# Optimization experiments

Measured on AMD Instinct MI355X. Metric: run time of the kernel, lower is better.

## Reference

```python
import jax, jax.numpy as jnp
import numpy as np

# Workspace layout (static slice bounds, per init_kwargs)
SS, SE = 0, 512        # spoke
HPS, HPE = 512, 768    # hub private
HSS, HSE = 768, 1024   # hub shared
TS, TE = 1024, 1088    # tag
HS, HE = 512, 1024     # full hub (priv + shared) for the read path

B, T, D_STATE, D_MODEL, D_LATENT = 8, 4096, 1088, 1024, 128


def setup_inputs() -> dict:
    key = jax.random.key(0)
    ks = jax.random.split(key, 10)
    scale = 0.02  # typical init scale for learned projections
    return {
        "S": jax.random.normal(ks[0], (B, T, D_STATE), jnp.float32),
        "w_spoke": jax.random.normal(ks[1], (B, T, SE - SS), jnp.float32),
        "w_hub_priv": jax.random.normal(ks[2], (B, T, HPE - HPS), jnp.float32),
        "w_hub_shared": jax.random.normal(ks[3], (B, T, HSE - HSS), jnp.float32),
        "tag": jax.random.normal(ks[4], (B, T, TE - TS), jnp.float32),
        "W_read": jax.random.normal(ks[5], (D_MODEL, D_STATE), jnp.float32) * scale,
        "cache": jnp.zeros((B, T, D_LATENT), jnp.float32),
        "latent": jax.random.normal(ks[6], (B, T, D_LATENT), jnp.float32),
        "Wk": jax.random.normal(ks[7], (D_MODEL, D_LATENT), jnp.float32) * scale,
        "Wv": jax.random.normal(ks[8], (D_MODEL, D_LATENT), jnp.float32) * scale,
    }


def reference(S, w_spoke, w_hub_priv, w_hub_shared, tag, W_read, cache, latent, Wk, Wv):
    # --- fused_workspace_write: four independent slice-adds into S ---
    S = S.at[:, :, SS:SE].add(w_spoke)
    S = S.at[:, :, HPS:HPE].add(w_hub_priv)
    S = S.at[:, :, HSS:HSE].add(w_hub_shared)
    S = S.at[:, :, TS:TE].add(tag)

    # --- fused_workspace_read: concat(spoke, hub, tag) then F.linear(., W_read) ---
    readable = jnp.concatenate(
        [S[:, :, SS:SE], S[:, :, HS:HE], S[:, :, TS:TE]], axis=-1
    )  # (B, T, D_STATE)
    out = jnp.einsum("btr,dr->btd", readable, W_read)  # (B, T, D_MODEL)

    # --- CWTLatentCache.update: overwrite latents at start_position=0 ---
    cache = jax.lax.dynamic_update_slice(cache, latent, (0, 0, 0))

    # --- K/V reconstruction from compressed latents via up-projections ---
    k = jnp.einsum("btl,dl->btd", cache, Wk)  # (B, T, D_MODEL)
    v = jnp.einsum("btl,dl->btd", cache, Wv)  # (B, T, D_MODEL)
    return (out, k, v)
```

## Files before the change

kernel.cpp:

```cpp
#include <hip/hip_runtime.h>

typedef __attribute__((ext_vector_type(8))) _Float16 half8;
typedef __attribute__((ext_vector_type(2))) __fp16 half2r;
typedef __attribute__((ext_vector_type(4))) float f32x4;

#define AS1 __attribute__((address_space(1)))
#define AS3 __attribute__((address_space(3)))

union H2U { half2r h; unsigned int u; };
union Frag { half8 v; unsigned long long d[2]; };

__device__ __forceinline__ unsigned int pk(float a, float b) {
    H2U x; x.h = __builtin_amdgcn_cvt_pkrtz(a, b); return x.u;
}

__device__ __forceinline__ void gload_lds16(const void* g, void* l) {
    __builtin_amdgcn_global_load_lds((const AS1 unsigned int*)g,
                                     (AS3 unsigned int*)l, 16, 0, 0);
}

#define WS2_OFF 2228224
#define WS2_SZ  524288
#define W2_ROWB 256
#define A16_SZ  71303168ull

__device__ __forceinline__ void pick_w(int ks, const float* wsp, const float* whp,
                                       const float* whs, const float* wtg,
                                       const float*& wbase, int& wstr, int& wko) {
    if (ks < 8)       { wbase = wsp; wstr = 512; wko = ks * 64; }
    else if (ks < 12) { wbase = whp; wstr = 256; wko = ks * 64 - 512; }
    else if (ks < 16) { wbase = whs; wstr = 256; wko = ks * 64 - 768; }
    else              { wbase = wtg; wstr = 64;  wko = 0; }
}

__device__ __forceinline__ size_t pf_addr(int r, int kt) {
    int kh = kt >> 5, k32 = kt & 31;
    int u = (k32 & 15) >> 2, pos8 = (k32 >> 4) << 3;
    return ((size_t)r << 7) + ((size_t)((((kh << 2) | u) ^ (r & 7)) << 4)) + pos8;
}

__global__ __launch_bounds__(256) void prep_w(const float* __restrict__ Wk,
                                              const float* __restrict__ Wv,
                                              char* __restrict__ ws) {
    int j = blockIdx.x * 256 + threadIdx.x;
    int r = j >> 5;
    int k = (j & 31) << 2;
    const float* src = (r < 1024) ? (Wk + (size_t)r * 128 + k)
                                  : (Wv + (size_t)(r - 1024) * 128 + k);
    f32x4 w = *(const f32x4*)src;
    uint2 q; q.x = pk(w.x, w.y); q.y = pk(w.z, w.w);
    size_t off = WS2_OFF + (size_t)r * W2_ROWB + ((k >> 6) << 7)
               + (((k & 63) << 1) ^ ((r & 7) << 4));
    *(uint2*)(ws + off) = q;
}

__device__ __forceinline__
void fuse_body(int u, const float* __restrict__ S, const float* __restrict__ wsp,
               const float* __restrict__ whp, const float* __restrict__ whs,
               const float* __restrict__ wtg, char* __restrict__ a16) {
    int row = u / 272;
    int rem = u % 272;
    int ks = rem >> 4;
    int k4 = (rem & 15) << 2;

    const float* wbase; int wstr, wko;
    pick_w(ks, wsp, whp, whs, wtg, wbase, wstr, wko);

    f32x4 s4 = *(const f32x4*)(S + (size_t)row * 1088 + ks * 64 + k4);
    f32x4 w4 = *(const f32x4*)(wbase + (size_t)row * wstr + wko + k4);
    uint2 q; q.x = pk(s4.x + w4.x, s4.y + w4.y);
             q.y = pk(s4.z + w4.z, s4.w + w4.w);
    size_t off = ((size_t)((row >> 7) * 17 + ks) << 14) + pf_addr(row & 127, k4);
    *(uint2*)(a16 + off) = q;
}

__device__ __forceinline__
void kv_body(int mblk, int nb, const float* __restrict__ lat,
             const char* __restrict__ ws2, float* __restrict__ outk,
             float* __restrict__ outv, char* lds) {
    char* Al = lds;
    char* Bl = lds + 16384;

    int m0 = mblk << 7;
    int nrow0 = nb << 7;
    float* out = (nb < 8) ? outk : outv;
    int n0 = (nb & 7) << 7;

    int tid = threadIdx.x;
    int lane = tid & 63, wid = tid >> 6;
    int wm = (wid >> 1) << 6, wn = (wid & 1) << 6;
    int lp = lane & 15, lg = lane >> 4;

    f32x4 acc[4][4] = {};

    for (int ks = 0; ks < 2; ++ks) {
        __syncthreads();
        {
            const char* wrow = ws2 + (size_t)nrow0 * W2_ROWB + ks * 128;
            #pragma unroll
            for (int c = 0; c < 4; ++c) {
                int s = c * 4096 + wid * 1024 + lane * 16;
                int n = s >> 7, cb = s & 127;
                gload_lds16(wrow + (size_t)n * W2_ROWB + cb,
                            Bl + c * 4096 + wid * 1024);
            }
        }
        #pragma unroll
        for (int i = 0; i < 8; ++i) {
            int u = i * 256 + tid;
            int row = u >> 4;
            int k4 = (u & 15) << 2;
            f32x4 s4 = *(const f32x4*)(lat + (size_t)(m0 + row) * 128 + ks * 64 + k4);
            uint2 q; q.x = pk(s4.x, s4.y); q.y = pk(s4.z, s4.w);
            *(uint2*)(Al + (row << 7) + ((k4 << 1) ^ ((row & 7) << 4))) = q;
        }
        __syncthreads();

        #pragma unroll
        for (int b = 0; b < 2; ++b) {
            Frag af[4], bf[4];
            #pragma unroll
            for (int f = 0; f < 4; ++f) {
                int ra = wm + f * 16 + lp;  int xa = (ra & 7) << 4;
                af[f].d[0] = *(const unsigned long long*)(Al + (ra << 7) + ((b * 64 + lg * 8) ^ xa));
                af[f].d[1] = *(const unsigned long long*)(Al + (ra << 7) + ((b * 64 + 32 + lg * 8) ^ xa));
                int rb = wn + f * 16 + lp;  int xb = (rb & 7) << 4;
                bf[f].d[0] = *(const unsigned long long*)(Bl + (rb << 7) + ((b * 64 + lg * 8) ^ xb));
                bf[f].d[1] = *(const unsigned long long*)(Bl + (rb << 7) + ((b * 64 + 32 + lg * 8) ^ xb));
            }
            #pragma unroll
            for (int i = 0; i < 4; ++i)
                #pragma unroll
                for (int j = 0; j < 4; ++j)
                    acc[i][j] = __builtin_amdgcn_mfma_f32_16x16x32_f16(af[i].v, bf[j].v, acc[i][j], 0, 0, 0);
        }
    }

    #pragma unroll
    for (int i = 0; i < 4; ++i)
        #pragma unroll
        for (int j = 0; j < 4; ++j) {
            int row = m0 + wm + i * 16 + (lg << 2);
            int col = n0 + wn + j * 16 + lp;
            float* p = out + (size_t)row * 1024 + col;
            #pragma unroll
            for (int r = 0; r < 4; ++r) p[(size_t)r * 1024] = acc[i][j][r];
        }
}

__global__ __launch_bounds__(256, 3)
void fuse_kv(const float* __restrict__ S, const float* __restrict__ wsp,
             const float* __restrict__ whp, const float* __restrict__ whs,
             const float* __restrict__ wtg, char* __restrict__ a16,
             const float* __restrict__ lat, const char* __restrict__ ws2,
             float* __restrict__ outk, float* __restrict__ outv,
             const float* __restrict__ Wr, char* __restrict__ ws,
             int kvpg, int gsz, int nmain) {
    __shared__ char lds[32768];
    int bid = blockIdx.x;
    if (bid >= nmain) {
        int id = (bid - nmain) * 256 + threadIdx.x;
        int n = id / 272;
        int k = (id % 272) * 4;
        f32x4 w = *(const f32x4*)(Wr + (size_t)n * 1088 + k);
        uint2 q; q.x = pk(w.x, w.y); q.y = pk(w.z, w.w);
        int t = k >> 6;
        size_t off = ((size_t)((n >> 7) * 17 + t) << 14) + pf_addr(n & 127, k & 63);
        *(uint2*)(ws + off) = q;
        return;
    }
    int g = bid / gsz, slot = bid - g * gsz;
    if (slot < 17) {
        fuse_body((g * 17 + slot) * 256 + threadIdx.x, S, wsp, whp, whs, wtg, a16);
    } else {
        int idx = g * kvpg + (slot - 17);
        int mblk, nb;
        if (kvpg == 2) { int wg = (idx & 7) * 512 + (idx >> 3); mblk = wg >> 4; nb = wg & 15; }
        else           { int wg = (idx & 7) * 256 + (idx >> 3); mblk = wg >> 3; nb = wg & 7; }
        kv_body(mblk, nb, lat, ws2, outk, outv, lds);
    }
}

__global__ __launch_bounds__(256, 3)
void gemm_v(const float* __restrict__ lat, const char* __restrict__ ws2,
            float* __restrict__ outk, float* __restrict__ outv) {
    __shared__ char lds[32768];
    int idx = blockIdx.x;
    int wg = (idx & 7) * 256 + (idx >> 3);
    kv_body(wg >> 3, 8 + (wg & 7), lat, ws2, outk, outv, lds);
}

__global__ __launch_bounds__(512, 2)
void gemm_read(const char* __restrict__ a16, const char* __restrict__ wws,
               float* __restrict__ out) {
    extern __shared__ char lds[];

    int bid = blockIdx.x;
    int wg   = (bid & 7) * 64 + (bid >> 3);
    int mblk = wg >> 2, nblk = wg & 3;
    int m0 = mblk << 8, n0 = nblk << 8;

    int tid = threadIdx.x;
    int lane = tid & 63, wid = tid >> 6;
    int wm = (wid >> 2) << 7, wn = (wid & 3) << 6;
    int lp = lane & 15, lg = lane >> 4;

    int aoff = (wid >> 2) * 16384;
    int boff = 32768 + (wn >> 7) * 16384;
    int cb64 = wn & 64;

    const char* srcH[4];
    srcH[0] = a16 + ((size_t)((m0 >> 7) * 17) << 14);
    srcH[1] = srcH[0] + (17 << 14);
    srcH[2] = wws + ((size_t)((n0 >> 7) * 17) << 14);
    srcH[3] = srcH[2] + (17 << 14);

    f32x4 acc[8][4] = {};
    Frag af[4], bf[4];

#define STAGE(T, H, DB) do {                                               \
        const char* s_ = srcH[H] + ((size_t)(T) << 14);                    \
        char* d_ = lds + (DB) + (H) * 16384;                               \
        gload_lds16(s_ + tid * 16, d_ + tid * 16);                         \
        gload_lds16(s_ + 8192 + tid * 16, d_ + 8192 + tid * 16);           \
    } while (0)

#define LOADA(MH, KH, BB) do {                                             \
        _Pragma("unroll")                                                  \
        for (int f = 0; f < 4; ++f) {                                      \
            int r_ = (MH) * 64 + f * 16 + lp;                              \
            af[f] = *(const Frag*)(lds + (BB) + aoff + (r_ << 7)           \
                     + ((((((KH) << 2) | lg) ^ (r_ & 7))) << 4));          \
        }                                                                  \
    } while (0)

#define LOADB(KH, BB) do {                                                 \
        _Pragma("unroll")                                                  \
        for (int g = 0; g < 4; ++g) {                                      \
            int c_ = cb64 + g * 16 + lp;                                   \
            bf[g] = *(const Frag*)(lds + (BB) + boff + (c_ << 7)           \
                     + ((((((KH) << 2) | lg) ^ (c_ & 7))) << 4));          \
        }                                                                  \
    } while (0)

#define MFMA16(MH) do {                                                    \
        __builtin_amdgcn_s_setprio(1);                                     \
        _Pragma("unroll")                                                  \
        for (int f = 0; f < 4; ++f)                                        \
            _Pragma("unroll")                                              \
            for (int g = 0; g < 4; ++g)                                    \
                acc[(MH) * 4 + f][g] = __builtin_amdgcn_mfma_f32_16x16x32_f16( \
                    af[f].v, bf[g].v, acc[(MH) * 4 + f][g], 0, 0, 0);      \
        __builtin_amdgcn_s_setprio(0);                                     \
    } while (0)

    STAGE(0, 0, 0); STAGE(0, 1, 0); STAGE(0, 2, 0); STAGE(0, 3, 0);

    for (int t = 0; t < 16; ++t) {
        int BB = (t & 1) << 16;
        int NB = BB ^ 65536;
        STAGE(t + 1, 0, NB);
        asm volatile("s_waitcnt vmcnt(2)" ::: "memory");
        __builtin_amdgcn_s_barrier();
        LOADB(0, BB); LOADA(0, 0, BB);
        MFMA16(0);
        __builtin_amdgcn_s_barrier();
        LOADA(1, 0, BB);
        STAGE(t + 1, 1, NB);
        __builtin_amdgcn_s_barrier();
        MFMA16(1);
        __builtin_amdgcn_s_barrier();
        LOADB(1, BB); LOADA(0, 1, BB);
        STAGE(t + 1, 2, NB);
        __builtin_amdgcn_s_barrier();
        MFMA16(0);
        __builtin_amdgcn_s_barrier();
        LOADA(1, 1, BB);
        STAGE(t + 1, 3, NB);
        __builtin_amdgcn_s_barrier();
        MFMA16(1);
        __builtin_amdgcn_s_barrier();
    }
    {
        const int BB = 0;
        asm volatile("s_waitcnt vmcnt(0)" ::: "memory");
        __builtin_amdgcn_s_barrier();
        LOADB(0, BB); LOADA(0, 0, BB); MFMA16(0);
        __builtin_amdgcn_s_barrier();
        LOADA(1, 0, BB); MFMA16(1);
        __builtin_amdgcn_s_barrier();
        LOADB(1, BB); LOADA(0, 1, BB); MFMA16(0);
        __builtin_amdgcn_s_barrier();
        LOADA(1, 1, BB); MFMA16(1);
    }

    #pragma unroll
    for (int i = 0; i < 8; ++i)
        #pragma unroll
        for (int j = 0; j < 4; ++j) {
            int row = m0 + wm + i * 16 + (lg << 2);
            int col = n0 + wn + j * 16 + lp;
            float* p = out + (size_t)row * 1024 + col;
            #pragma unroll
            for (int r = 0; r < 4; ++r) p[(size_t)r * 1024] = acc[i][j][r];
        }
#undef STAGE
#undef LOADA
#undef LOADB
#undef MFMA16
}

extern "C" void kernel_launch(void* const* d_in, const int* in_sizes, int n_in,
                              void* d_out, int out_size, void* d_ws, size_t ws_size,
                              hipStream_t stream) {
    const float* S   = (const float*)d_in[0];
    const float* wsp = (const float*)d_in[1];
    const float* whp = (const float*)d_in[2];
    const float* whs = (const float*)d_in[3];
    const float* wtg = (const float*)d_in[4];
    const float* Wr  = (const float*)d_in[5];
    const float* lat = (const float*)d_in[7];
    const float* Wk  = (const float*)d_in[8];
    const float* Wv  = (const float*)d_in[9];
    float* out = (float*)d_out;
    char*  ws  = (char*)d_ws;

    float* outk = out + 33554432ull;
    float* outv = out + 67108864ull;

    static bool lds_init = false;
    if (!lds_init) {
        hipFuncSetAttribute(reinterpret_cast<const void*>(gemm_read),
                            hipFuncAttributeMaxDynamicSharedMemorySize, 131072);
        lds_init = true;
    }

    const size_t A16_WS_OFF = (size_t)WS2_OFF + WS2_SZ;
    const size_t ws_need = A16_WS_OFF + A16_SZ;

    hipLaunchKernelGGL(prep_w, dim3(256), dim3(256), 0, stream, Wk, Wv, ws);

    if (ws_size >= ws_need) {
        char* a16 = ws + A16_WS_OFF;
        int nmain = 2048 * 19;
        hipLaunchKernelGGL(fuse_kv, dim3(nmain + 1088), dim3(256), 0, stream,
                           S, wsp, whp, whs, wtg, a16,
                           lat, ws + WS2_OFF, outk, outv, Wr, ws, 2, 19, nmain);
        hipLaunchKernelGGL(gemm_read, dim3(512), dim3(512), 131072, stream,
                           a16, ws, out);
    } else {
        char* a16 = (char*)outv;
        int nmain = 2048 * 18;
        hipLaunchKernelGGL(fuse_kv, dim3(nmain + 1088), dim3(256), 0, stream,
                           S, wsp, whp, whs, wtg, a16,
                           lat, ws + WS2_OFF, outk, outv, Wr, ws, 1, 18, nmain);
        hipLaunchKernelGGL(gemm_read, dim3(512), dim3(512), 131072, stream,
                           a16, ws, out);
        hipLaunchKernelGGL(gemm_v, dim3(2048), dim3(256), 0, stream,
                           lat, ws + WS2_OFF, outk, outv);
    }
}
```

Before: 229.2 us.

## Move K GEMM tiles into read GEMM launch to balance work across kernels

The fused write/convert kernel now handles only the V up-projection tiles, not both K and V. The K up-projection tiles are interleaved into a new combined read-GEMM kernel: two of every three blocks each run two 256-thread K tiles side by side in separate LDS halves. The goal is to shorten the memory-bound first kernel and fill idle compute during the read GEMM. The risk is that the 512-thread, 128KB-LDS launch configuration limits occupancy for the small K tiles, and mixing tile types may unbalance the schedule.

```diff
diff --git a/kernel.cpp b/kernel.cpp
--- a/kernel.cpp
+++ b/kernel.cpp
@@ -77,7 +77,7 @@
 __device__ __forceinline__
 void kv_body(int mblk, int nb, const float* __restrict__ lat,
              const char* __restrict__ ws2, float* __restrict__ outk,
-             float* __restrict__ outv, char* lds) {
+             float* __restrict__ outv, char* lds, int tid) {
     char* Al = lds;
     char* Bl = lds + 16384;
 
@@ -86,7 +86,6 @@
     float* out = (nb < 8) ? outk : outv;
     int n0 = (nb & 7) << 7;
 
-    int tid = threadIdx.x;
     int lane = tid & 63, wid = tid >> 6;
     int wm = (wid >> 1) << 6, wn = (wid & 1) << 6;
     int lp = lane & 15, lg = lane >> 4;
@@ -155,7 +154,7 @@
              const float* __restrict__ lat, const char* __restrict__ ws2,
              float* __restrict__ outk, float* __restrict__ outv,
              const float* __restrict__ Wr, char* __restrict__ ws,
-             int kvpg, int gsz, int nmain) {
+             int kvpg, int gsz, int nmain, int nb_off) {
     __shared__ char lds[32768];
     int bid = blockIdx.x;
     if (bid >= nmain) {
@@ -176,8 +175,8 @@
         int idx = g * kvpg + (slot - 17);
         int mblk, nb;
         if (kvpg == 2) { int wg = (idx & 7) * 512 + (idx >> 3); mblk = wg >> 4; nb = wg & 15; }
-        else           { int wg = (idx & 7) * 256 + (idx >> 3); mblk = wg >> 3; nb = wg & 7; }
-        kv_body(mblk, nb, lat, ws2, outk, outv, lds);
+        else           { int wg = (idx & 7) * 256 + (idx >> 3); mblk = wg >> 3; nb = nb_off + (wg & 7); }
+        kv_body(mblk, nb, lat, ws2, outk, outv, lds, threadIdx.x);
     }
 }
 
@@ -187,16 +186,13 @@
     __shared__ char lds[32768];
     int idx = blockIdx.x;
     int wg = (idx & 7) * 256 + (idx >> 3);
-    kv_body(wg >> 3, 8 + (wg & 7), lat, ws2, outk, outv, lds);
-}
-
-__global__ __launch_bounds__(512, 2)
-void gemm_read(const char* __restrict__ a16, const char* __restrict__ wws,
-               float* __restrict__ out) {
-    extern __shared__ char lds[];
-
-    int bid = blockIdx.x;
-    int wg   = (bid & 7) * 64 + (bid >> 3);
+    kv_body(wg >> 3, 8 + (wg & 7), lat, ws2, outk, outv, lds, threadIdx.x);
+}
+
+__device__ __forceinline__
+void read_body(int idx, const char* __restrict__ a16, const char* __restrict__ wws,
+               float* __restrict__ out, char* lds) {
+    int wg   = (idx & 7) * 64 + (idx >> 3);
     int mblk = wg >> 2, nblk = wg & 3;
     int m0 = mblk << 8, n0 = nblk << 8;
 
@@ -308,6 +304,31 @@
 #undef LOADA
 #undef LOADB
 #undef MFMA16
+}
+
+__global__ __launch_bounds__(512, 2)
+void gemm_read(const char* __restrict__ a16, const char* __restrict__ wws,
+               float* __restrict__ out) {
+    extern __shared__ char lds[];
+    read_body(blockIdx.x, a16, wws, out, lds);
+}
+
+__global__ __launch_bounds__(512, 2)
+void gemm_read_k(const char* __restrict__ a16, const char* __restrict__ wws,
+                 float* __restrict__ out, const float* __restrict__ lat,
+                 const char* __restrict__ ws2, float* __restrict__ outk) {
+    extern __shared__ char lds[];
+    int bid = blockIdx.x;
+    int g = bid / 3, s = bid - g * 3;
+    if (s == 0) {
+        read_body(g, a16, wws, out, lds);
+    } else {
+        int j = g * 2 + (s - 1);
+        int half = threadIdx.x >> 8;
+        int t = 2 * j + half;
+        kv_body(t >> 3, t & 7, lat, ws2, outk, outk,
+                lds + half * 32768, threadIdx.x & 255);
+    }
 }
 
 extern "C" void kernel_launch(void* const* d_in, const int* in_sizes, int n_in,
@@ -332,6 +353,8 @@
     if (!lds_init) {
         hipFuncSetAttribute(reinterpret_cast<const void*>(gemm_read),
                             hipFuncAttributeMaxDynamicSharedMemorySize, 131072);
+        hipFuncSetAttribute(reinterpret_cast<const void*>(gemm_read_k),
+                            hipFuncAttributeMaxDynamicSharedMemorySize, 131072);
         lds_init = true;
     }
 
@@ -342,18 +365,18 @@
 
     if (ws_size >= ws_need) {
         char* a16 = ws + A16_WS_OFF;
-        int nmain = 2048 * 19;
+        int nmain = 2048 * 18;
         hipLaunchKernelGGL(fuse_kv, dim3(nmain + 1088), dim3(256), 0, stream,
                            S, wsp, whp, whs, wtg, a16,
-                           lat, ws + WS2_OFF, outk, outv, Wr, ws, 2, 19, nmain);
-        hipLaunchKernelGGL(gemm_read, dim3(512), dim3(512), 131072, stream,
-                           a16, ws, out);
+                           lat, ws + WS2_OFF, outk, outv, Wr, ws, 1, 18, nmain, 8);
+        hipLaunchKernelGGL(gemm_read_k, dim3(1536), dim3(512), 131072, stream,
+                           a16, ws, out, lat, ws + WS2_OFF, outk);
     } else {
         char* a16 = (char*)outv;
         int nmain = 2048 * 18;
         hipLaunchKernelGGL(fuse_kv, dim3(nmain + 1088), dim3(256), 0, stream,
                            S, wsp, whp, whs, wtg, a16,
-                           lat, ws + WS2_OFF, outk, outv, Wr, ws, 1, 18, nmain);
+                           lat, ws + WS2_OFF, outk, outv, Wr, ws, 1, 18, nmain, 0);
         hipLaunchKernelGGL(gemm_read, dim3(512), dim3(512), 131072, stream,
                            a16, ws, out);
         hipLaunchKernelGGL(gemm_v, dim3(2048), dim3(256), 0, stream,
```

After: 263.0 us. 14.7% more time.
